# Optimization experiments

Hardware: AMD Instinct MI355X
Metric: run time of the kernel (lower is better)

## Reference

```python
import jax, jax.numpy as jnp
import numpy as np

N = 50000
E = 500000
D = 128      # input_nf = output_nf = hidden_nf
EPS = 1e-8
MAX_TRANS = 10.0


def setup_inputs() -> dict:
    key = jax.random.key(0)
    ks = jax.random.split(key, 16)
    s = lambda k, shp: jax.random.normal(k, shp, dtype=jnp.float32) * 0.05
    inp = {
        "h": jax.random.normal(ks[0], (N, D), dtype=jnp.float32),
        "edge_index": jax.random.randint(ks[1], (2, E), 0, N, dtype=jnp.int64),
        "coord": jax.random.normal(ks[2], (N, 3), dtype=jnp.float32),
        # edge_mlp: Linear(2D+1 -> D), SiLU, Linear(D -> D), SiLU
        "We1": s(ks[3], (2 * D + 1, D)), "be1": jnp.zeros((D,), jnp.float32),
        "We2": s(ks[4], (D, D)),         "be2": jnp.zeros((D,), jnp.float32),
        # att_mlp: Linear(D -> 1), Sigmoid
        "Watt": s(ks[5], (D, 1)), "batt": jnp.zeros((1,), jnp.float32),
        # coord_mlp: Linear(D -> D), SiLU, Linear(D -> 1, bias=False, xavier gain=0.001)
        "Wc1": s(ks[6], (D, D)), "bc1": jnp.zeros((D,), jnp.float32),
        "Wc2": s(ks[7], (D, 1)) * 0.001,
        # node_mlp: Linear(2D -> D), SiLU, Linear(D -> D)
        "Wn1": s(ks[8], (2 * D, D)), "bn1": jnp.zeros((D,), jnp.float32),
        "Wn2": s(ks[9], (D, D)),     "bn2": jnp.zeros((D,), jnp.float32),
    }
    return inp


def _segment_mean(data, seg_ids, num_segments):
    tot = jax.ops.segment_sum(data, seg_ids, num_segments=num_segments)
    cnt = jax.ops.segment_sum(jnp.ones_like(data), seg_ids, num_segments=num_segments)
    return tot / jnp.clip(cnt, 1.0, None)


def reference(h, edge_index, coord, We1, be1, We2, be2, Watt, batt,
              Wc1, bc1, Wc2, Wn1, bn1, Wn2, bn2):
    row, col = edge_index[0], edge_index[1]

    # coord2radial (normalize=False)
    coord_diff = coord[row] - coord[col]                      # [E, 3]
    radial = jnp.sum(coord_diff ** 2, axis=1, keepdims=True)  # [E, 1]

    # edge_model with attention
    e_in = jnp.concatenate([h[row], h[col], radial], axis=1)  # [E, 2D+1]
    e = jax.nn.silu(e_in @ We1 + be1)
    edge_feat = jax.nn.silu(e @ We2 + be2)                    # [E, D]
    att = jax.nn.sigmoid(edge_feat @ Watt + batt)             # [E, 1]
    edge_feat = edge_feat * att

    # coord_model (update_coords=True, coords_agg='mean', tanh=False)
    cw = jax.nn.silu(edge_feat @ Wc1 + bc1) @ Wc2             # [E, 1]
    trans = jnp.clip(coord_diff * cw, -MAX_TRANS, MAX_TRANS)  # [E, 3]
    agg_c = jnp.clip(_segment_mean(trans, row, N), -MAX_TRANS, MAX_TRANS)
    coord_out = coord + agg_c

    # node_model (residual=True)
    agg = jax.ops.segment_sum(edge_feat, row, num_segments=N)  # [N, D]
    n_in = jnp.concatenate([h, agg], axis=1)                   # [N, 2D]
    h_out = h + (jax.nn.silu(n_in @ Wn1 + bn1) @ Wn2 + bn2)

    return h_out, coord_out, edge_feat
```

## Files before the change

kernel.cpp:

```cpp
#include <hip/hip_runtime.h>

typedef unsigned short ushort_t;
typedef __attribute__((ext_vector_type(8))) short short8;
typedef __attribute__((ext_vector_type(4))) float f32x4;

#define NN 50000
#define EE 500000
#define DD 128
#define MAXT 10.0f

#define MFMA(a,b,c) __builtin_amdgcn_mfma_f32_16x16x32_bf16((a),(b),(c),0,0,0)

__device__ __forceinline__ ushort_t f2bf(float x){
  unsigned u = __float_as_uint(x);
  u += 0x7FFFu + ((u>>16)&1u);
  return (ushort_t)(u>>16);
}
__device__ __forceinline__ float sigm(float x){ return 1.0f/(1.0f+__expf(-x)); }
__device__ __forceinline__ float siluf(float x){ return x*sigm(x); }
__device__ __forceinline__ float clamp10(float x){ return fminf(fmaxf(x,-MAXT),MAXT); }

__device__ __forceinline__ short8 ldcvt(const float* p){
  f32x4 x = *(const f32x4*)p;
  f32x4 y = *(const f32x4*)(p+4);
  short8 t;
  #pragma unroll
  for (int j=0;j<4;++j){ t[j]=(short)f2bf(x[j]); t[j+4]=(short)f2bf(y[j]); }
  return t;
}

__global__ void k_prep(const float* __restrict__ We1, const float* __restrict__ We2,
                       const float* __restrict__ Wc1, const float* __restrict__ Wn1,
                       const float* __restrict__ Wn2, ushort_t* __restrict__ wpre)
{
  int idx = blockIdx.x*256 + threadIdx.x;
  if (idx >= 7*16384) return;
  int mat = idx >> 14;
  int loc = idx & 16383;
  int n = loc >> 7;
  int kidx = loc & 127;
  int ko = 16*(kidx&7) + (kidx>>3);
  float v;
  switch(mat){
    case 0: v = We1[kidx*DD + n]; break;
    case 1: v = We1[(128+kidx)*DD + n]; break;
    case 2: v = We2[ko*DD + n]; break;
    case 3: v = Wc1[ko*DD + n]; break;
    case 4: v = Wn1[kidx*DD + n]; break;
    case 5: v = Wn1[(128+kidx)*DD + n]; break;
    default: v = Wn2[ko*DD + n]; break;
  }
  int byteoff = n*256 + ((kidx*2) ^ ((n&7)<<4));
  *(ushort_t*)((char*)wpre + (size_t)mat*32768 + byteoff) = f2bf(v);
}

__global__ void k_zero(int* __restrict__ cnt){
  int i = blockIdx.x*256 + threadIdx.x;
  if (i < NN) cnt[i] = 0;
}
__global__ void k_count(const int* __restrict__ eidx, int* __restrict__ cnt){
  int e = blockIdx.x*256 + threadIdx.x;
  if (e < EE) atomicAdd(&cnt[eidx[e]], 1);
}
__global__ void k_scan(const int* __restrict__ cnt, int* __restrict__ rowstart,
                       int* __restrict__ cursor)
{
  __shared__ int part[1024];
  const int t = threadIdx.x;
  const int C = 49;
  int c0 = t*C, c1 = min(c0+C, NN);
  int sum = 0;
  for (int i=c0;i<c1;++i) sum += cnt[i];
  part[t] = sum; __syncthreads();
  for (int off=1; off<1024; off<<=1){
    int v = (t>=off)? part[t-off] : 0;
    __syncthreads();
    part[t] += v;
    __syncthreads();
  }
  int run = (t>0)? part[t-1] : 0;
  for (int i=c0;i<c1;++i){ rowstart[i]=run; cursor[i]=run; run += cnt[i]; }
  if (t==0) rowstart[NN] = EE;
}
__global__ void k_scatter(const int* __restrict__ eidx, int* __restrict__ cursor,
                          int* __restrict__ csr){
  int e = blockIdx.x*256 + threadIdx.x;
  if (e < EE){
    int p = atomicAdd(&cursor[eidx[e]], 1);
    csr[p] = e;
  }
}

__device__ __forceinline__ void gemm_lds(const ushort_t* ebuf, const ushort_t* Wbuf,
                                         int wv, int q, int s, f32x4 acc[2][8])
{
  #pragma unroll
  for (int kc=0;kc<4;++kc){
    const int koff = ((kc*64+q*16) ^ ((s&7)<<4));
    short8 a0 = *(const short8*)((const char*)ebuf + (wv*32+s)*256    + koff);
    short8 a1 = *(const short8*)((const char*)ebuf + (wv*32+16+s)*256 + koff);
    #pragma unroll
    for (int ct=0;ct<8;++ct){
      short8 bf = *(const short8*)((const char*)Wbuf + (ct*16+s)*256 + koff);
      acc[0][ct] = MFMA(a0,bf,acc[0][ct]);
      acc[1][ct] = MFMA(a1,bf,acc[1][ct]);
    }
  }
}
__device__ __forceinline__ void gemm_regA(const short8 af[2][4], const ushort_t* Wbuf,
                                          int q, int s, f32x4 acc[2][8])
{
  #pragma unroll
  for (int kc=0;kc<4;++kc){
    const int koff = ((kc*64+q*16) ^ ((s&7)<<4));
    #pragma unroll
    for (int ct=0;ct<8;++ct){
      short8 bf = *(const short8*)((const char*)Wbuf + (ct*16+s)*256 + koff);
      acc[0][ct] = MFMA(af[0][kc],bf,acc[0][ct]);
      acc[1][ct] = MFMA(af[1][kc],bf,acc[1][ct]);
    }
  }
}
__device__ __forceinline__ void zacc(f32x4 acc[2][8]){
  #pragma unroll
  for (int a=0;a<2;++a)
    #pragma unroll
    for (int b=0;b<8;++b) acc[a][b] = (f32x4){0.f,0.f,0.f,0.f};
}

__launch_bounds__(256,2)
__global__ void k_edge(const float* __restrict__ h,
                       const int* __restrict__ eidx,
                       const float* __restrict__ coord,
                       const float* __restrict__ We1,
                       const float* __restrict__ be1,
                       const float* __restrict__ be2,
                       const float* __restrict__ Watt,
                       const float* __restrict__ batt,
                       const float* __restrict__ bc1,
                       const float* __restrict__ Wc2,
                       const ushort_t* __restrict__ wpre,
                       float* __restrict__ ef_out,
                       float* __restrict__ trans)
{
  __shared__ ushort_t Wbuf[16384];
  __shared__ ushort_t ebuf[16384];
  const int tid = threadIdx.x;
  const int wv = tid>>6, ln = tid&63;
  const int q = ln>>4, s = ln&15;
  const int we0 = blockIdx.x*128 + wv*32;
  const int* rowI = eidx;
  const int* colI = eidx + EE;

  const int eM = min(we0 + (ln&31), EE-1);
  const int rM = rowI[eM], cM = colI[eM];
  const float cdx = coord[rM*3+0]-coord[cM*3+0];
  const float cdy = coord[rM*3+1]-coord[cM*3+1];
  const float cdz = coord[rM*3+2]-coord[cM*3+2];
  const float radial = cdx*cdx+cdy*cdy+cdz*cdz;

  const int eS0 = min(we0 + s,      EE-1);
  const int eS1 = min(we0 + 16 + s, EE-1);
  const int nR0 = rowI[eS0], nR1 = rowI[eS1];
  const int nC0 = colI[eS0], nC1 = colI[eS1];

  f32x4 acc[2][8];
  zacc(acc);
  short8 af[2][4];

  #pragma unroll
  for (int kc=0;kc<4;++kc){
    af[0][kc] = ldcvt(h + (size_t)nR0*DD + kc*32 + q*8);
    af[1][kc] = ldcvt(h + (size_t)nR1*DD + kc*32 + q*8);
  }
  { const f32x4* src=(const f32x4*)(wpre); f32x4* dst=(f32x4*)Wbuf;
    #pragma unroll
    for(int i=0;i<8;++i) dst[tid+256*i]=src[tid+256*i]; }
  __syncthreads();
  gemm_regA(af, Wbuf, q, s, acc);

  #pragma unroll
  for (int kc=0;kc<4;++kc){
    af[0][kc] = ldcvt(h + (size_t)nC0*DD + kc*32 + q*8);
    af[1][kc] = ldcvt(h + (size_t)nC1*DD + kc*32 + q*8);
  }
  __syncthreads();
  { const f32x4* src=(const f32x4*)(wpre+16384); f32x4* dst=(f32x4*)Wbuf;
    #pragma unroll
    for(int i=0;i<8;++i) dst[tid+256*i]=src[tid+256*i]; }
  __syncthreads();
  gemm_regA(af, Wbuf, q, s, acc);

  {
    float wr[8], bb[8];
    #pragma unroll
    for (int t=0;t<8;++t){ wr[t]=We1[256*DD + 16*t+s]; bb[t]=be1[16*t+s]; }
    #pragma unroll
    for (int mt=0;mt<2;++mt)
      #pragma unroll
      for (int r=0;r<4;++r){
        int mloc = mt*16 + q*4 + r;
        float rad = __shfl(radial, mloc);
        short8 pk;
        #pragma unroll
        for (int t=0;t<8;++t){
          float v = siluf(acc[mt][t][r] + rad*wr[t] + bb[t]);
          pk[t]=(short)f2bf(v);
        }
        int m = wv*32 + mloc;
        *(short8*)((char*)ebuf + m*256 + ((s*16) ^ ((m&7)<<4))) = pk;
      }
  }
  zacc(acc);
  __syncthreads();
  { const f32x4* src=(const f32x4*)(wpre+2*16384); f32x4* dst=(f32x4*)Wbuf;
    #pragma unroll
    for(int i=0;i<8;++i) dst[tid+256*i]=src[tid+256*i]; }
  __syncthreads();

  gemm_lds(ebuf, Wbuf, wv, q, s, acc);
  {
    float wa[8], bb[8];
    #pragma unroll
    for (int t=0;t<8;++t){ wa[t]=Watt[16*t+s]; bb[t]=be2[16*t+s]; }
    const float bat = batt[0];
    #pragma unroll
    for (int mt=0;mt<2;++mt)
      #pragma unroll
      for (int r=0;r<4;++r){
        #pragma unroll
        for (int t=0;t<8;++t) acc[mt][t][r] = siluf(acc[mt][t][r] + bb[t]);
        float p=0.f;
        #pragma unroll
        for (int t=0;t<8;++t) p += acc[mt][t][r]*wa[t];
        p += __shfl_xor(p,1); p += __shfl_xor(p,2);
        p += __shfl_xor(p,4); p += __shfl_xor(p,8);
        const float att = sigm(p + bat);
        #pragma unroll
        for (int t=0;t<8;++t) acc[mt][t][r] *= att;
      }
    #pragma unroll
    for (int mt=0;mt<2;++mt)
      #pragma unroll
      for (int r=0;r<4;++r){
        int mloc = mt*16+q*4+r;
        int e = we0 + mloc;
        short8 pk;
        #pragma unroll
        for (int t=0;t<8;++t){
          float v = acc[mt][t][r];
          pk[t]=(short)f2bf(v);
          if (e < EE) ef_out[(size_t)e*DD + 16*t+s] = v;
        }
        int m = wv*32+mloc;
        *(short8*)((char*)ebuf + m*256 + ((s*16) ^ ((m&7)<<4))) = pk;
      }
  }
  zacc(acc);
  __syncthreads();
  { const f32x4* src=(const f32x4*)(wpre+3*16384); f32x4* dst=(f32x4*)Wbuf;
    #pragma unroll
    for(int i=0;i<8;++i) dst[tid+256*i]=src[tid+256*i]; }
  __syncthreads();

  gemm_lds(ebuf, Wbuf, wv, q, s, acc);
  {
    float wc[8], bb[8];
    #pragma unroll
    for (int t=0;t<8;++t){ wc[t]=Wc2[16*t+s]; bb[t]=bc1[16*t+s]; }
    #pragma unroll
    for (int mt=0;mt<2;++mt)
      #pragma unroll
      for (int r=0;r<4;++r){
        float p=0.f;
        #pragma unroll
        for (int t=0;t<8;++t) p += siluf(acc[mt][t][r]+bb[t])*wc[t];
        p += __shfl_xor(p,1); p += __shfl_xor(p,2);
        p += __shfl_xor(p,4); p += __shfl_xor(p,8);
        int mloc = mt*16+q*4+r;
        int e = we0+mloc;
        float dx = __shfl(cdx, mloc), dy = __shfl(cdy, mloc), dz = __shfl(cdz, mloc);
        if (e < EE && s == 0){
          trans[(size_t)e*3+0] = clamp10(dx*p);
          trans[(size_t)e*3+1] = clamp10(dy*p);
          trans[(size_t)e*3+2] = clamp10(dz*p);
        }
      }
  }
}

__launch_bounds__(256)
__global__ void k_agg(const float* __restrict__ ef,
                      const float* __restrict__ trans,
                      const int* __restrict__ rowstart,
                      const int* __restrict__ csr,
                      const float* __restrict__ coord,
                      float* __restrict__ agg,
                      float* __restrict__ coord_out)
{
  const int wv = threadIdx.x>>6, ln = threadIdx.x&63;
  const int n = blockIdx.x*4 + wv;
  if (n >= NN) return;
  const int rs = rowstart[n], re = rowstart[n+1];
  const int deg = re - rs;
  const int half = ln>>5, l4 = (ln&31)*4;
  float a0=0,a1=0,a2=0,a3=0;
  for (int j=half; j<deg; j+=2){
    const float* p = ef + (size_t)csr[rs+j]*DD + l4;
    f32x4 v = *(const f32x4*)p;
    a0+=v[0]; a1+=v[1]; a2+=v[2]; a3+=v[3];
  }
  a0 += __shfl_xor(a0,32); a1 += __shfl_xor(a1,32);
  a2 += __shfl_xor(a2,32); a3 += __shfl_xor(a3,32);
  if (half==0){
    f32x4 o = {a0,a1,a2,a3};
    *(f32x4*)(agg + (size_t)n*DD + l4) = o;
  }
  float tx=0,ty=0,tz=0;
  for (int j=ln;j<deg;j+=64){
    const float* t = trans + (size_t)csr[rs+j]*3;
    tx+=t[0]; ty+=t[1]; tz+=t[2];
  }
  #pragma unroll
  for (int m=1;m<64;m<<=1){
    tx+=__shfl_xor(tx,m); ty+=__shfl_xor(ty,m); tz+=__shfl_xor(tz,m);
  }
  if (ln==0){
    const float inv = 1.0f/(float)max(deg,1);
    coord_out[(size_t)n*3+0] = coord[(size_t)n*3+0] + clamp10(tx*inv);
    coord_out[(size_t)n*3+1] = coord[(size_t)n*3+1] + clamp10(ty*inv);
    coord_out[(size_t)n*3+2] = coord[(size_t)n*3+2] + clamp10(tz*inv);
  }
}

__launch_bounds__(256,2)
__global__ void k_node(const float* __restrict__ h,
                       const float* __restrict__ agg,
                       const ushort_t* __restrict__ wpre,
                       const float* __restrict__ bn1,
                       const float* __restrict__ bn2,
                       float* __restrict__ hout)
{
  __shared__ ushort_t Wbuf[16384];
  __shared__ ushort_t ubuf[16384];
  const int tid = threadIdx.x;
  const int wv = tid>>6, ln = tid&63;
  const int q = ln>>4, s = ln&15;
  const int n0 = blockIdx.x*128 + wv*32;
  const int nd0 = min(n0 + s,      NN-1);
  const int nd1 = min(n0 + 16 + s, NN-1);

  f32x4 acc[2][8];
  zacc(acc);
  short8 af[2][4];

  #pragma unroll
  for (int kc=0;kc<4;++kc){
    af[0][kc] = ldcvt(h + (size_t)nd0*DD + kc*32 + q*8);
    af[1][kc] = ldcvt(h + (size_t)nd1*DD + kc*32 + q*8);
  }
  { const f32x4* src=(const f32x4*)(wpre+4*16384); f32x4* dst=(f32x4*)Wbuf;
    #pragma unroll
    for(int i=0;i<8;++i) dst[tid+256*i]=src[tid+256*i]; }
  __syncthreads();
  gemm_regA(af, Wbuf, q, s, acc);

  #pragma unroll
  for (int kc=0;kc<4;++kc){
    af[0][kc] = ldcvt(agg + (size_t)nd0*DD + kc*32 + q*8);
    af[1][kc] = ldcvt(agg + (size_t)nd1*DD + kc*32 + q*8);
  }
  __syncthreads();
  { const f32x4* src=(const f32x4*)(wpre+5*16384); f32x4* dst=(f32x4*)Wbuf;
    #pragma unroll
    for(int i=0;i<8;++i) dst[tid+256*i]=src[tid+256*i]; }
  __syncthreads();
  gemm_regA(af, Wbuf, q, s, acc);

  {
    float bb[8];
    #pragma unroll
    for (int t=0;t<8;++t) bb[t]=bn1[16*t+s];
    #pragma unroll
    for (int mt=0;mt<2;++mt)
      #pragma unroll
      for (int r=0;r<4;++r){
        int mloc = mt*16+q*4+r;
        short8 pk;
        #pragma unroll
        for (int t=0;t<8;++t) pk[t]=(short)f2bf(siluf(acc[mt][t][r]+bb[t]));
        int m = wv*32+mloc;
        *(short8*)((char*)ubuf + m*256 + ((s*16) ^ ((m&7)<<4))) = pk;
      }
  }
  zacc(acc);
  __syncthreads();
  { const f32x4* src=(const f32x4*)(wpre+6*16384); f32x4* dst=(f32x4*)Wbuf;
    #pragma unroll
    for(int i=0;i<8;++i) dst[tid+256*i]=src[tid+256*i]; }
  __syncthreads();

  gemm_lds(ubuf, Wbuf, wv, q, s, acc);

  {
    float bb[8];
    #pragma unroll
    for (int t=0;t<8;++t) bb[t]=bn2[16*t+s];
    #pragma unroll
    for (int mt=0;mt<2;++mt)
      #pragma unroll
      for (int r=0;r<4;++r){
        int n = n0 + mt*16 + q*4 + r;
        if (n < NN){
          #pragma unroll
          for (int t=0;t<8;++t){
            int c = 16*t+s;
            hout[(size_t)n*DD+c] = h[(size_t)n*DD+c] + acc[mt][t][r] + bb[t];
          }
        }
      }
  }
}

extern "C" void kernel_launch(void* const* d_in, const int* in_sizes, int n_in,
                              void* d_out, int out_size, void* d_ws, size_t ws_size,
                              hipStream_t stream)
{
  const float* h    = (const float*)d_in[0];
  const int*   eidx = (const int*)  d_in[1];
  const float* coord= (const float*)d_in[2];
  const float* We1  = (const float*)d_in[3];
  const float* be1  = (const float*)d_in[4];
  const float* We2  = (const float*)d_in[5];
  const float* be2  = (const float*)d_in[6];
  const float* Watt = (const float*)d_in[7];
  const float* batt = (const float*)d_in[8];
  const float* Wc1  = (const float*)d_in[9];
  const float* bc1  = (const float*)d_in[10];
  const float* Wc2  = (const float*)d_in[11];
  const float* Wn1  = (const float*)d_in[12];
  const float* bn1  = (const float*)d_in[13];
  const float* Wn2  = (const float*)d_in[14];
  const float* bn2  = (const float*)d_in[15];

  float* hout     = (float*)d_out;
  float* coordout = hout + (size_t)NN*DD;
  float* efout    = coordout + (size_t)NN*3;

  char* ws = (char*)d_ws;
  float* trans   = (float*)(ws);
  float* agg     = (float*)(ws + 6000000);
  int*   cnt     = (int*)  (ws + 31600000);
  int*   cursor  = (int*)  (ws + 31800000);
  int*   rowstart= (int*)  (ws + 32000000);
  int*   csr     = (int*)  (ws + 32200064);
  ushort_t* wpre = (ushort_t*)(ws + 34200064);

  k_prep   <<<448, 256, 0, stream>>>(We1, We2, Wc1, Wn1, Wn2, wpre);
  k_zero   <<<196, 256, 0, stream>>>(cnt);
  k_count  <<<1954,256, 0, stream>>>(eidx, cnt);
  k_scan   <<<1,  1024, 0, stream>>>(cnt, rowstart, cursor);
  k_scatter<<<1954,256, 0, stream>>>(eidx, cursor, csr);
  k_edge   <<<3907,256, 0, stream>>>(h, eidx, coord, We1, be1, be2, Watt, batt,
                                     bc1, Wc2, wpre, efout, trans);
  k_agg    <<<12500,256,0, stream>>>(efout, trans, rowstart, csr, coord, agg, coordout);
  k_node   <<<391, 256, 0, stream>>>(h, agg, wpre, bn1, bn2, hout);
}
```

Before: 768.3 us.

## Parallelize CSR scan across blocks and use 512-thread blocks with 16 rows per wave

Replaces the single-block serial scan over 50000 counts with a three-kernel block-sum, block-offset and per-block scan. The edge and node kernels move from 256-thread blocks with 32 rows per wave to 512-thread blocks with 16 rows per wave, which halves accumulator registers per thread to allow more resident waves. The trade-off is that each B-fragment read from LDS now feeds one MFMA instead of two, so the LDS traffic per unit of matrix work doubles. bsum and boff reuse the csr buffer as scratch before the scatter overwrites it.

```diff
diff --git a/kernel.cpp b/kernel.cpp
--- a/kernel.cpp
+++ b/kernel.cpp
@@ -62,25 +62,49 @@
   int e = blockIdx.x*256 + threadIdx.x;
   if (e < EE) atomicAdd(&cnt[eidx[e]], 1);
 }
-__global__ void k_scan(const int* __restrict__ cnt, int* __restrict__ rowstart,
-                       int* __restrict__ cursor)
-{
-  __shared__ int part[1024];
-  const int t = threadIdx.x;
-  const int C = 49;
-  int c0 = t*C, c1 = min(c0+C, NN);
-  int sum = 0;
-  for (int i=c0;i<c1;++i) sum += cnt[i];
-  part[t] = sum; __syncthreads();
-  for (int off=1; off<1024; off<<=1){
-    int v = (t>=off)? part[t-off] : 0;
+#define SCAN_B 196
+__global__ void k_bsum(const int* __restrict__ cnt, int* __restrict__ bsum){
+  __shared__ int sh[256];
+  int t = threadIdx.x;
+  int i = blockIdx.x*256 + t;
+  sh[t] = (i < NN) ? cnt[i] : 0;
+  __syncthreads();
+  for (int off=128; off>0; off>>=1){
+    if (t < off) sh[t] += sh[t+off];
     __syncthreads();
-    part[t] += v;
+  }
+  if (t==0) bsum[blockIdx.x] = sh[0];
+}
+__global__ void k_bscan(const int* __restrict__ bsum, int* __restrict__ boff){
+  __shared__ int sh[256];
+  int t = threadIdx.x;
+  sh[t] = (t < SCAN_B) ? bsum[t] : 0;
+  __syncthreads();
+  for (int off=1; off<256; off<<=1){
+    int x = (t>=off) ? sh[t-off] : 0;
     __syncthreads();
-  }
-  int run = (t>0)? part[t-1] : 0;
-  for (int i=c0;i<c1;++i){ rowstart[i]=run; cursor[i]=run; run += cnt[i]; }
-  if (t==0) rowstart[NN] = EE;
+    sh[t] += x;
+    __syncthreads();
+  }
+  if (t < SCAN_B) boff[t] = (t>0) ? sh[t-1] : 0;
+}
+__global__ void k_rscan(const int* __restrict__ cnt, const int* __restrict__ boff,
+                        int* __restrict__ rowstart, int* __restrict__ cursor){
+  __shared__ int sh[256];
+  int t = threadIdx.x;
+  int i = blockIdx.x*256 + t;
+  int v = (i < NN) ? cnt[i] : 0;
+  sh[t] = v;
+  __syncthreads();
+  for (int off=1; off<256; off<<=1){
+    int x = (t>=off) ? sh[t-off] : 0;
+    __syncthreads();
+    sh[t] += x;
+    __syncthreads();
+  }
+  int excl = sh[t] - v + boff[blockIdx.x];
+  if (i < NN){ rowstart[i] = excl; cursor[i] = excl; }
+  if (i == 0) rowstart[NN] = EE;
 }
 __global__ void k_scatter(const int* __restrict__ eidx, int* __restrict__ cursor,
                           int* __restrict__ csr){
@@ -91,24 +115,22 @@
   }
 }
 
-__device__ __forceinline__ void gemm_lds(const ushort_t* ebuf, const ushort_t* Wbuf,
-                                         int wv, int q, int s, f32x4 acc[2][8])
+__device__ __forceinline__ void gemm_lds8(const ushort_t* ebuf, const ushort_t* Wbuf,
+                                          int wv, int q, int s, f32x4 acc[8])
 {
   #pragma unroll
   for (int kc=0;kc<4;++kc){
     const int koff = ((kc*64+q*16) ^ ((s&7)<<4));
-    short8 a0 = *(const short8*)((const char*)ebuf + (wv*32+s)*256    + koff);
-    short8 a1 = *(const short8*)((const char*)ebuf + (wv*32+16+s)*256 + koff);
+    short8 a0 = *(const short8*)((const char*)ebuf + (wv*16+s)*256 + koff);
     #pragma unroll
     for (int ct=0;ct<8;++ct){
       short8 bf = *(const short8*)((const char*)Wbuf + (ct*16+s)*256 + koff);
-      acc[0][ct] = MFMA(a0,bf,acc[0][ct]);
-      acc[1][ct] = MFMA(a1,bf,acc[1][ct]);
-    }
-  }
-}
-__device__ __forceinline__ void gemm_regA(const short8 af[2][4], const ushort_t* Wbuf,
-                                          int q, int s, f32x4 acc[2][8])
+      acc[ct] = MFMA(a0,bf,acc[ct]);
+    }
+  }
+}
+__device__ __forceinline__ void gemm_regA8(const short8 af[4], const ushort_t* Wbuf,
+                                           int q, int s, f32x4 acc[8])
 {
   #pragma unroll
   for (int kc=0;kc<4;++kc){
@@ -116,19 +138,16 @@
     #pragma unroll
     for (int ct=0;ct<8;++ct){
       short8 bf = *(const short8*)((const char*)Wbuf + (ct*16+s)*256 + koff);
-      acc[0][ct] = MFMA(af[0][kc],bf,acc[0][ct]);
-      acc[1][ct] = MFMA(af[1][kc],bf,acc[1][ct]);
-    }
-  }
-}
-__device__ __forceinline__ void zacc(f32x4 acc[2][8]){
-  #pragma unroll
-  for (int a=0;a<2;++a)
-    #pragma unroll
-    for (int b=0;b<8;++b) acc[a][b] = (f32x4){0.f,0.f,0.f,0.f};
-}
-
-__launch_bounds__(256,2)
+      acc[ct] = MFMA(af[kc],bf,acc[ct]);
+    }
+  }
+}
+__device__ __forceinline__ void zacc8(f32x4 acc[8]){
+  #pragma unroll
+  for (int b=0;b<8;++b) acc[b] = (f32x4){0.f,0.f,0.f,0.f};
+}
+
+__launch_bounds__(512,4)
 __global__ void k_edge(const float* __restrict__ h,
                        const int* __restrict__ eidx,
                        const float* __restrict__ coord,
@@ -148,144 +167,131 @@
   const int tid = threadIdx.x;
   const int wv = tid>>6, ln = tid&63;
   const int q = ln>>4, s = ln&15;
-  const int we0 = blockIdx.x*128 + wv*32;
+  const int we0 = blockIdx.x*128 + wv*16;
   const int* rowI = eidx;
   const int* colI = eidx + EE;
 
-  const int eM = min(we0 + (ln&31), EE-1);
+  const int eM = min(we0 + (ln&15), EE-1);
   const int rM = rowI[eM], cM = colI[eM];
   const float cdx = coord[rM*3+0]-coord[cM*3+0];
   const float cdy = coord[rM*3+1]-coord[cM*3+1];
   const float cdz = coord[rM*3+2]-coord[cM*3+2];
   const float radial = cdx*cdx+cdy*cdy+cdz*cdz;
 
-  const int eS0 = min(we0 + s,      EE-1);
-  const int eS1 = min(we0 + 16 + s, EE-1);
-  const int nR0 = rowI[eS0], nR1 = rowI[eS1];
-  const int nC0 = colI[eS0], nC1 = colI[eS1];
-
-  f32x4 acc[2][8];
-  zacc(acc);
-  short8 af[2][4];
-
-  #pragma unroll
-  for (int kc=0;kc<4;++kc){
-    af[0][kc] = ldcvt(h + (size_t)nR0*DD + kc*32 + q*8);
-    af[1][kc] = ldcvt(h + (size_t)nR1*DD + kc*32 + q*8);
-  }
+  const int eS0 = min(we0 + s, EE-1);
+  const int nR0 = rowI[eS0], nC0 = colI[eS0];
+
+  f32x4 acc[8];
+  zacc8(acc);
+  short8 af[4];
+
+  #pragma unroll
+  for (int kc=0;kc<4;++kc)
+    af[kc] = ldcvt(h + (size_t)nR0*DD + kc*32 + q*8);
   { const f32x4* src=(const f32x4*)(wpre); f32x4* dst=(f32x4*)Wbuf;
     #pragma unroll
-    for(int i=0;i<8;++i) dst[tid+256*i]=src[tid+256*i]; }
-  __syncthreads();
-  gemm_regA(af, Wbuf, q, s, acc);
-
-  #pragma unroll
-  for (int kc=0;kc<4;++kc){
-    af[0][kc] = ldcvt(h + (size_t)nC0*DD + kc*32 + q*8);
-    af[1][kc] = ldcvt(h + (size_t)nC1*DD + kc*32 + q*8);
-  }
+    for(int i=0;i<4;++i) dst[tid+512*i]=src[tid+512*i]; }
+  __syncthreads();
+  gemm_regA8(af, Wbuf, q, s, acc);
+
+  #pragma unroll
+  for (int kc=0;kc<4;++kc)
+    af[kc] = ldcvt(h + (size_t)nC0*DD + kc*32 + q*8);
   __syncthreads();
   { const f32x4* src=(const f32x4*)(wpre+16384); f32x4* dst=(f32x4*)Wbuf;
     #pragma unroll
-    for(int i=0;i<8;++i) dst[tid+256*i]=src[tid+256*i]; }
-  __syncthreads();
-  gemm_regA(af, Wbuf, q, s, acc);
+    for(int i=0;i<4;++i) dst[tid+512*i]=src[tid+512*i]; }
+  __syncthreads();
+  gemm_regA8(af, Wbuf, q, s, acc);
 
   {
     float wr[8], bb[8];
     #pragma unroll
     for (int t=0;t<8;++t){ wr[t]=We1[256*DD + 16*t+s]; bb[t]=be1[16*t+s]; }
     #pragma unroll
-    for (int mt=0;mt<2;++mt)
-      #pragma unroll
-      for (int r=0;r<4;++r){
-        int mloc = mt*16 + q*4 + r;
-        float rad = __shfl(radial, mloc);
-        short8 pk;
-        #pragma unroll
-        for (int t=0;t<8;++t){
-          float v = siluf(acc[mt][t][r] + rad*wr[t] + bb[t]);
-          pk[t]=(short)f2bf(v);
-        }
-        int m = wv*32 + mloc;
-        *(short8*)((char*)ebuf + m*256 + ((s*16) ^ ((m&7)<<4))) = pk;
+    for (int r=0;r<4;++r){
+      int mloc = q*4 + r;
+      float rad = __shfl(radial, mloc);
+      short8 pk;
+      #pragma unroll
+      for (int t=0;t<8;++t){
+        float v = siluf(acc[t][r] + rad*wr[t] + bb[t]);
+        pk[t]=(short)f2bf(v);
       }
-  }
-  zacc(acc);
+      int m = wv*16 + mloc;
+      *(short8*)((char*)ebuf + m*256 + ((s*16) ^ ((m&7)<<4))) = pk;
+    }
+  }
+  zacc8(acc);
   __syncthreads();
   { const f32x4* src=(const f32x4*)(wpre+2*16384); f32x4* dst=(f32x4*)Wbuf;
     #pragma unroll
-    for(int i=0;i<8;++i) dst[tid+256*i]=src[tid+256*i]; }
-  __syncthreads();
-
-  gemm_lds(ebuf, Wbuf, wv, q, s, acc);
+    for(int i=0;i<4;++i) dst[tid+512*i]=src[tid+512*i]; }
+  __syncthreads();
+
+  gemm_lds8(ebuf, Wbuf, wv, q, s, acc);
   {
     float wa[8], bb[8];
     #pragma unroll
     for (int t=0;t<8;++t){ wa[t]=Watt[16*t+s]; bb[t]=be2[16*t+s]; }
     const float bat = batt[0];
     #pragma unroll
-    for (int mt=0;mt<2;++mt)
-      #pragma unroll
-      for (int r=0;r<4;++r){
+    for (int r=0;r<4;++r){
+      #pragma unroll
+      for (int t=0;t<8;++t) acc[t][r] = siluf(acc[t][r] + bb[t]);
+      float p=0.f;
+      #pragma unroll
+      for (int t=0;t<8;++t) p += acc[t][r]*wa[t];
+      p += __shfl_xor(p,1); p += __shfl_xor(p,2);
+      p += __shfl_xor(p,4); p += __shfl_xor(p,8);
+      const float att = sigm(p + bat);
+      #pragma unroll
+      for (int t=0;t<8;++t) acc[t][r] *= att;
+    }
+    #pragma unroll
+    for (int r=0;r<4;++r){
+      int mloc = q*4 + r;
+      int e = we0 + mloc;
+      short8 pk;
+      #pragma unroll
+      for (int t=0;t<8;++t) pk[t]=(short)f2bf(acc[t][r]);
+      int m = wv*16 + mloc;
+      *(short8*)((char*)ebuf + m*256 + ((s*16) ^ ((m&7)<<4))) = pk;
+      if (e < EE){
+        float* rp = ef_out + (size_t)e*DD + s;
         #pragma unroll
-        for (int t=0;t<8;++t) acc[mt][t][r] = siluf(acc[mt][t][r] + bb[t]);
-        float p=0.f;
-        #pragma unroll
-        for (int t=0;t<8;++t) p += acc[mt][t][r]*wa[t];
-        p += __shfl_xor(p,1); p += __shfl_xor(p,2);
-        p += __shfl_xor(p,4); p += __shfl_xor(p,8);
-        const float att = sigm(p + bat);
-        #pragma unroll
-        for (int t=0;t<8;++t) acc[mt][t][r] *= att;
+        for (int t=0;t<8;++t) rp[16*t] = acc[t][r];
       }
-    #pragma unroll
-    for (int mt=0;mt<2;++mt)
-      #pragma unroll
-      for (int r=0;r<4;++r){
-        int mloc = mt*16+q*4+r;
-        int e = we0 + mloc;
-        short8 pk;
-        #pragma unroll
-        for (int t=0;t<8;++t){
-          float v = acc[mt][t][r];
-          pk[t]=(short)f2bf(v);
-          if (e < EE) ef_out[(size_t)e*DD + 16*t+s] = v;
-        }
-        int m = wv*32+mloc;
-        *(short8*)((char*)ebuf + m*256 + ((s*16) ^ ((m&7)<<4))) = pk;
-      }
-  }
-  zacc(acc);
+    }
+  }
+  zacc8(acc);
   __syncthreads();
   { const f32x4* src=(const f32x4*)(wpre+3*16384); f32x4* dst=(f32x4*)Wbuf;
     #pragma unroll
-    for(int i=0;i<8;++i) dst[tid+256*i]=src[tid+256*i]; }
-  __syncthreads();
-
-  gemm_lds(ebuf, Wbuf, wv, q, s, acc);
+    for(int i=0;i<4;++i) dst[tid+512*i]=src[tid+512*i]; }
+  __syncthreads();
+
+  gemm_lds8(ebuf, Wbuf, wv, q, s, acc);
   {
     float wc[8], bb[8];
     #pragma unroll
     for (int t=0;t<8;++t){ wc[t]=Wc2[16*t+s]; bb[t]=bc1[16*t+s]; }
     #pragma unroll
-    for (int mt=0;mt<2;++mt)
-      #pragma unroll
-      for (int r=0;r<4;++r){
-        float p=0.f;
-        #pragma unroll
-        for (int t=0;t<8;++t) p += siluf(acc[mt][t][r]+bb[t])*wc[t];
-        p += __shfl_xor(p,1); p += __shfl_xor(p,2);
-        p += __shfl_xor(p,4); p += __shfl_xor(p,8);
-        int mloc = mt*16+q*4+r;
-        int e = we0+mloc;
-        float dx = __shfl(cdx, mloc), dy = __shfl(cdy, mloc), dz = __shfl(cdz, mloc);
-        if (e < EE && s == 0){
-          trans[(size_t)e*3+0] = clamp10(dx*p);
-          trans[(size_t)e*3+1] = clamp10(dy*p);
-          trans[(size_t)e*3+2] = clamp10(dz*p);
-        }
+    for (int r=0;r<4;++r){
+      float p=0.f;
+      #pragma unroll
+      for (int t=0;t<8;++t) p += siluf(acc[t][r]+bb[t])*wc[t];
+      p += __shfl_xor(p,1); p += __shfl_xor(p,2);
+      p += __shfl_xor(p,4); p += __shfl_xor(p,8);
+      int mloc = q*4 + r;
+      int e = we0 + mloc;
+      float dx = __shfl(cdx, mloc), dy = __shfl(cdy, mloc), dz = __shfl(cdz, mloc);
+      if (e < EE && s == 0){
+        trans[(size_t)e*3+0] = clamp10(dx*p);
+        trans[(size_t)e*3+1] = clamp10(dy*p);
+        trans[(size_t)e*3+2] = clamp10(dz*p);
       }
+    }
   }
 }
 
@@ -333,7 +339,7 @@
   }
 }
 
-__launch_bounds__(256,2)
+__launch_bounds__(512,4)
 __global__ void k_node(const float* __restrict__ h,
                        const float* __restrict__ agg,
                        const ushort_t* __restrict__ wpre,
@@ -346,79 +352,69 @@
   const int tid = threadIdx.x;
   const int wv = tid>>6, ln = tid&63;
   const int q = ln>>4, s = ln&15;
-  const int n0 = blockIdx.x*128 + wv*32;
-  const int nd0 = min(n0 + s,      NN-1);
-  const int nd1 = min(n0 + 16 + s, NN-1);
-
-  f32x4 acc[2][8];
-  zacc(acc);
-  short8 af[2][4];
-
-  #pragma unroll
-  for (int kc=0;kc<4;++kc){
-    af[0][kc] = ldcvt(h + (size_t)nd0*DD + kc*32 + q*8);
-    af[1][kc] = ldcvt(h + (size_t)nd1*DD + kc*32 + q*8);
-  }
+  const int n0 = blockIdx.x*128 + wv*16;
+  const int nd0 = min(n0 + s, NN-1);
+
+  f32x4 acc[8];
+  zacc8(acc);
+  short8 af[4];
+
+  #pragma unroll
+  for (int kc=0;kc<4;++kc)
+    af[kc] = ldcvt(h + (size_t)nd0*DD + kc*32 + q*8);
   { const f32x4* src=(const f32x4*)(wpre+4*16384); f32x4* dst=(f32x4*)Wbuf;
     #pragma unroll
-    for(int i=0;i<8;++i) dst[tid+256*i]=src[tid+256*i]; }
-  __syncthreads();
-  gemm_regA(af, Wbuf, q, s, acc);
-
-  #pragma unroll
-  for (int kc=0;kc<4;++kc){
-    af[0][kc] = ldcvt(agg + (size_t)nd0*DD + kc*32 + q*8);
-    af[1][kc] = ldcvt(agg + (size_t)nd1*DD + kc*32 + q*8);
-  }
+    for(int i=0;i<4;++i) dst[tid+512*i]=src[tid+512*i]; }
+  __syncthreads();
+  gemm_regA8(af, Wbuf, q, s, acc);
+
+  #pragma unroll
+  for (int kc=0;kc<4;++kc)
+    af[kc] = ldcvt(agg + (size_t)nd0*DD + kc*32 + q*8);
   __syncthreads();
   { const f32x4* src=(const f32x4*)(wpre+5*16384); f32x4* dst=(f32x4*)Wbuf;
     #pragma unroll
-    for(int i=0;i<8;++i) dst[tid+256*i]=src[tid+256*i]; }
-  __syncthreads();
-  gemm_regA(af, Wbuf, q, s, acc);
+    for(int i=0;i<4;++i) dst[tid+512*i]=src[tid+512*i]; }
+  __syncthreads();
+  gemm_regA8(af, Wbuf, q, s, acc);
 
   {
     float bb[8];
     #pragma unroll
     for (int t=0;t<8;++t) bb[t]=bn1[16*t+s];
     #pragma unroll
-    for (int mt=0;mt<2;++mt)
-      #pragma unroll
-      for (int r=0;r<4;++r){
-        int mloc = mt*16+q*4+r;
-        short8 pk;
-        #pragma unroll
-        for (int t=0;t<8;++t) pk[t]=(short)f2bf(siluf(acc[mt][t][r]+bb[t]));
-        int m = wv*32+mloc;
-        *(short8*)((char*)ubuf + m*256 + ((s*16) ^ ((m&7)<<4))) = pk;
-      }
-  }
-  zacc(acc);
+    for (int r=0;r<4;++r){
+      int mloc = q*4 + r;
+      short8 pk;
+      #pragma unroll
+      for (int t=0;t<8;++t) pk[t]=(short)f2bf(siluf(acc[t][r]+bb[t]));
+      int m = wv*16 + mloc;
+      *(short8*)((char*)ubuf + m*256 + ((s*16) ^ ((m&7)<<4))) = pk;
+    }
+  }
+  zacc8(acc);
   __syncthreads();
   { const f32x4* src=(const f32x4*)(wpre+6*16384); f32x4* dst=(f32x4*)Wbuf;
     #pragma unroll
-    for(int i=0;i<8;++i) dst[tid+256*i]=src[tid+256*i]; }
-  __syncthreads();
-
-  gemm_lds(ubuf, Wbuf, wv, q, s, acc);
+    for(int i=0;i<4;++i) dst[tid+512*i]=src[tid+512*i]; }
+  __syncthreads();
+
+  gemm_lds8(ubuf, Wbuf, wv, q, s, acc);
 
   {
     float bb[8];
     #pragma unroll
     for (int t=0;t<8;++t) bb[t]=bn2[16*t+s];
     #pragma unroll
-    for (int mt=0;mt<2;++mt)
-      #pragma unroll
-      for (int r=0;r<4;++r){
-        int n = n0 + mt*16 + q*4 + r;
-        if (n < NN){
-          #pragma unroll
-          for (int t=0;t<8;++t){
-            int c = 16*t+s;
-            hout[(size_t)n*DD+c] = h[(size_t)n*DD+c] + acc[mt][t][r] + bb[t];
-          }
-        }
+    for (int r=0;r<4;++r){
+      int n = n0 + q*4 + r;
+      if (n < NN){
+        const float* hp = h + (size_t)n*DD + s;
+        float* op = hout + (size_t)n*DD + s;
+        #pragma unroll
+        for (int t=0;t<8;++t) op[16*t] = hp[16*t] + acc[t][r] + bb[t];
       }
+    }
   }
 }
 
@@ -455,14 +451,18 @@
   int*   rowstart= (int*)  (ws + 32000000);
   int*   csr     = (int*)  (ws + 32200064);
   ushort_t* wpre = (ushort_t*)(ws + 34200064);
+  int*   bsum    = csr;
+  int*   boff    = csr + 256;
 
   k_prep   <<<448, 256, 0, stream>>>(We1, We2, Wc1, Wn1, Wn2, wpre);
   k_zero   <<<196, 256, 0, stream>>>(cnt);
   k_count  <<<1954,256, 0, stream>>>(eidx, cnt);
-  k_scan   <<<1,  1024, 0, stream>>>(cnt, rowstart, cursor);
+  k_bsum   <<<196, 256, 0, stream>>>(cnt, bsum);
+  k_bscan  <<<1,   256, 0, stream>>>(bsum, boff);
+  k_rscan  <<<196, 256, 0, stream>>>(cnt, boff, rowstart, cursor);
   k_scatter<<<1954,256, 0, stream>>>(eidx, cursor, csr);
-  k_edge   <<<3907,256, 0, stream>>>(h, eidx, coord, We1, be1, be2, Watt, batt,
+  k_edge   <<<3907,512, 0, stream>>>(h, eidx, coord, We1, be1, be2, Watt, batt,
                                      bc1, Wc2, wpre, efout, trans);
   k_agg    <<<12500,256,0, stream>>>(efout, trans, rowstart, csr, coord, agg, coordout);
-  k_node   <<<391, 256, 0, stream>>>(h, agg, wpre, bn1, bn2, hout);
-}
+  k_node   <<<391, 512, 0, stream>>>(h, agg, wpre, bn1, bn2, hout);
+}
```

After: 661.4 us. -13.9%, faster.
